# Performance work log

Hardware: AMD Instinct MI355X
Metric: run time of the kernel (lower is better)

Reference implementation:

```python
import jax, jax.numpy as jnp
import numpy as np

N_NODES = 100000


def _sage_conv(x, src, dst, W_l, b_l, W_r):
    # mean-aggregate neighbor (source) features at target nodes
    gathered = x[src]                                   # [E, D]
    summed = jax.ops.segment_sum(gathered, dst, num_segments=N_NODES)  # [N, D]
    deg = jax.ops.segment_sum(jnp.ones((src.shape[0],), x.dtype), dst,
                              num_segments=N_NODES)     # [N]
    mean = summed / jnp.maximum(deg, 1.0)[:, None]      # zero stays zero for isolated nodes
    # PyG SAGEConv: lin_l(aggr) + lin_r(x); bias on lin_l only
    return mean @ W_l + b_l + x @ W_r


def setup_inputs() -> dict:
    key = jax.random.key(0)
    ks = jax.random.split(key, 9)
    x = jax.random.normal(ks[0], (N_NODES, 128), dtype=jnp.float32)
    edge_index = jax.random.randint(ks[1], (2, 1600000), 0, N_NODES, dtype=jnp.int64)
    s1 = 1.0 / np.sqrt(128.0)
    s2 = 1.0 / np.sqrt(32.0)
    return {
        "x": x,
        "edge_index": edge_index,
        "W1_l": jax.random.normal(ks[2], (128, 32), jnp.float32) * s1,
        "b1_l": jax.random.normal(ks[3], (32,), jnp.float32) * s1,
        "W1_r": jax.random.normal(ks[4], (128, 32), jnp.float32) * s1,
        "W2_l": jax.random.normal(ks[5], (32, 32), jnp.float32) * s2,
        "b2_l": jax.random.normal(ks[6], (32,), jnp.float32) * s2,
        "W2_r": jax.random.normal(ks[7], (32, 32), jnp.float32) * s2,
    }


def reference(x, edge_index, W1_l, b1_l, W1_r, W2_l, b2_l, W2_r):
    src, dst = edge_index[0], edge_index[1]
    h = _sage_conv(x, src, dst, W1_l, b1_l, W1_r)
    h = jax.nn.relu(h)
    # dropout is identity in eval mode
    h = _sage_conv(h, src, dst, W2_l, b2_l, W2_r)
    return jax.nn.relu(h)
```

## Files before the change

### kernel.cpp

```cpp
#include <hip/hip_runtime.h>


typedef _Float16 f16;
typedef _Float16 f16x4 __attribute__((ext_vector_type(4)));
typedef _Float16 half8 __attribute__((ext_vector_type(8)));
typedef float f32x4 __attribute__((ext_vector_type(4)));

#define MAXBINS 2048
#define SHIFT 6
#define BINSZ 64
#define CAP 48
#define BSTR 52
#define GBI 3392
#define GSC 256
#define BSC 512
#define SRC_BITS 17
#define SRC_MASK 0x1FFFFu
#define XSTRIDE 136


__global__ __launch_bounds__(256) void gemm_mfma(const float* __restrict__ x,
                                                 const float* __restrict__ Wl,
                                                 const float* __restrict__ Wr,
                                                 f16* __restrict__ yl,
                                                 float* __restrict__ yr,
                                                 int N) {
    __shared__ __align__(16) f16 sX[64 * XSTRIDE];
    __shared__ __align__(16) f16 sWT[64 * XSTRIDE];
    const int tid = threadIdx.x;
    const int row0 = blockIdx.x * 64;

    for (int i = tid; i < 64 * 32; i += 256) {
        int r = i >> 5, c4 = i & 31;
        int row = row0 + r;
        float4 v = make_float4(0.f, 0.f, 0.f, 0.f);
        if (row < N) v = *(const float4*)(x + (size_t)row * 128 + c4 * 4);
        f16* d = &sX[r * XSTRIDE + c4 * 4];
        d[0] = (f16)v.x; d[1] = (f16)v.y; d[2] = (f16)v.z; d[3] = (f16)v.w;
    }
    for (int i = tid; i < 64 * 128; i += 256) {
        int k = i >> 6, n = i & 63;
        float v = (n < 32) ? Wl[k * 32 + n] : Wr[k * 32 + (n - 32)];
        sWT[n * XSTRIDE + k] = (f16)v;
    }
    __syncthreads();

    const int w = tid >> 6;
    const int lane = tid & 63;
    const int l15 = lane & 15, quad = lane >> 4;
    f32x4 acc[4] = {};
#pragma unroll
    for (int kc = 0; kc < 4; ++kc) {
        half8 af = *(const half8*)&sX[(w * 16 + l15) * XSTRIDE + kc * 32 + quad * 8];
#pragma unroll
        for (int nt = 0; nt < 4; ++nt) {
            half8 bf = *(const half8*)&sWT[(nt * 16 + l15) * XSTRIDE + kc * 32 + quad * 8];
            acc[nt] = __builtin_amdgcn_mfma_f32_16x16x32_f16(af, bf, acc[nt], 0, 0, 0);
        }
    }
#pragma unroll
    for (int nt = 0; nt < 4; ++nt) {
        int c = nt * 16 + l15;
#pragma unroll
        for (int r = 0; r < 4; ++r) {
            int g = row0 + w * 16 + quad * 4 + r;
            if (c < 32) yl[(size_t)g * 32 + c] = (f16)acc[nt][r];
            else        yr[(size_t)g * 32 + (c - 32)] = acc[nt][r];
        }
    }
}


__global__ __launch_bounds__(BSC) void scatter_sort(const int* __restrict__ src,
                                                    const int* __restrict__ dst,
                                                    unsigned* __restrict__ pairs,
                                                    unsigned* __restrict__ binSeg,
                                                    int E, int chunk) {
    __shared__ int cnt[MAXBINS];
    __shared__ int wsum[8];
    const int tid = threadIdx.x;
    const int sb = blockIdx.x;
    for (int i = tid; i < MAXBINS; i += BSC) cnt[i] = 0;
    __syncthreads();

    const int base = sb * chunk;
    const int endE = base + chunk < E ? base + chunk : E;
    const int len = endE > base ? endE - base : 0;
    const int nv = len >> 2;
    const int rem = len & 3;
    const int4* s4 = (const int4*)(src + base);
    const int4* d4 = (const int4*)(dst + base);

    for (int i = tid; i < nv; i += BSC) {
        int4 d = d4[i];
        atomicAdd(&cnt[d.x >> SHIFT], 1);
        atomicAdd(&cnt[d.y >> SHIFT], 1);
        atomicAdd(&cnt[d.z >> SHIFT], 1);
        atomicAdd(&cnt[d.w >> SHIFT], 1);
    }
    if (tid < rem) atomicAdd(&cnt[dst[base + nv * 4 + tid] >> SHIFT], 1);
    __syncthreads();

    {
        int b0 = cnt[4 * tid], b1 = cnt[4 * tid + 1],
            b2 = cnt[4 * tid + 2], b3 = cnt[4 * tid + 3];
        int tsum = b0 + b1 + b2 + b3;
        const int lane = tid & 63, wave = tid >> 6;
        int incl = tsum;
#pragma unroll
        for (int off = 1; off < 64; off <<= 1) {
            int t = __shfl_up(incl, off, 64);
            if (lane >= off) incl += t;
        }
        if (lane == 63) wsum[wave] = incl;
        __syncthreads();
        if (tid == 0) {
            int a = 0;
#pragma unroll
            for (int w = 0; w < 8; ++w) { int t = wsum[w]; wsum[w] = a; a += t; }
        }
        __syncthreads();
        int ex = (incl - tsum) + wsum[wave];
        int e0 = ex, e1 = ex + b0, e2 = e1 + b1, e3 = e2 + b2;
        binSeg[(size_t)(4 * tid) * GSC + sb]     = ((unsigned)e0 << 16) | (unsigned)b0;
        binSeg[(size_t)(4 * tid + 1) * GSC + sb] = ((unsigned)e1 << 16) | (unsigned)b1;
        binSeg[(size_t)(4 * tid + 2) * GSC + sb] = ((unsigned)e2 << 16) | (unsigned)b2;
        binSeg[(size_t)(4 * tid + 3) * GSC + sb] = ((unsigned)e3 << 16) | (unsigned)b3;
        __syncthreads();
        cnt[4 * tid] = e0; cnt[4 * tid + 1] = e1;
        cnt[4 * tid + 2] = e2; cnt[4 * tid + 3] = e3;
    }
    __syncthreads();

    unsigned* out = pairs + (size_t)sb * chunk;
    for (int i = tid; i < nv; i += BSC) {
        int4 s = s4[i];
        int4 d = d4[i];
        int slot;
        slot = atomicAdd(&cnt[d.x >> SHIFT], 1);
        out[slot] = ((unsigned)(d.x & (BINSZ - 1)) << SRC_BITS) | (unsigned)s.x;
        slot = atomicAdd(&cnt[d.y >> SHIFT], 1);
        out[slot] = ((unsigned)(d.y & (BINSZ - 1)) << SRC_BITS) | (unsigned)s.y;
        slot = atomicAdd(&cnt[d.z >> SHIFT], 1);
        out[slot] = ((unsigned)(d.z & (BINSZ - 1)) << SRC_BITS) | (unsigned)s.z;
        slot = atomicAdd(&cnt[d.w >> SHIFT], 1);
        out[slot] = ((unsigned)(d.w & (BINSZ - 1)) << SRC_BITS) | (unsigned)s.w;
    }
    if (tid < rem) {
        int e = base + nv * 4 + tid;
        int s = src[e], d = dst[e];
        int slot = atomicAdd(&cnt[d >> SHIFT], 1);
        out[slot] = ((unsigned)(d & (BINSZ - 1)) << SRC_BITS) | (unsigned)s;
    }
}


__device__ __forceinline__ void build_bucket(const unsigned* __restrict__ pairs,
                                             const unsigned* __restrict__ binSeg,
                                             int* sBucket, int* sCnt,
                                             int b, int tid, int chunk) {
    unsigned dsc = binSeg[(size_t)b * GSC + tid];
    int scnt = (int)(dsc & 0xFFFFu);
    const unsigned* p = pairs + (size_t)tid * chunk + (dsc >> 16);
    int k = 0;
    for (; k + 4 <= scnt; k += 4) {
        unsigned p0 = p[k], p1 = p[k + 1], p2 = p[k + 2], p3 = p[k + 3];
        int l, s;
        l = p0 >> SRC_BITS; s = atomicAdd(&sCnt[l], 1);
        if (s < CAP) sBucket[l * BSTR + s] = (int)(p0 & SRC_MASK);
        l = p1 >> SRC_BITS; s = atomicAdd(&sCnt[l], 1);
        if (s < CAP) sBucket[l * BSTR + s] = (int)(p1 & SRC_MASK);
        l = p2 >> SRC_BITS; s = atomicAdd(&sCnt[l], 1);
        if (s < CAP) sBucket[l * BSTR + s] = (int)(p2 & SRC_MASK);
        l = p3 >> SRC_BITS; s = atomicAdd(&sCnt[l], 1);
        if (s < CAP) sBucket[l * BSTR + s] = (int)(p3 & SRC_MASK);
    }
    for (; k < scnt; ++k) {
        unsigned pk = p[k];
        int l = pk >> SRC_BITS;
        int s = atomicAdd(&sCnt[l], 1);
        if (s < CAP) sBucket[l * BSTR + s] = (int)(pk & SRC_MASK);
    }
}

#define PULL8(BKP, TBL, AX)                                                  \
    {                                                                        \
        int4 eA = (BKP)[0], eB = (BKP)[1];                                   \
        half8 v0 = *(const half8*)((TBL) + (size_t)eA.x * 32);               \
        half8 v1 = *(const half8*)((TBL) + (size_t)eA.y * 32);               \
        half8 v2 = *(const half8*)((TBL) + (size_t)eA.z * 32);               \
        half8 v3 = *(const half8*)((TBL) + (size_t)eA.w * 32);               \
        half8 w0 = *(const half8*)((TBL) + (size_t)eB.x * 32);               \
        half8 w1 = *(const half8*)((TBL) + (size_t)eB.y * 32);               \
        half8 w2 = *(const half8*)((TBL) + (size_t)eB.z * 32);               \
        half8 w3 = *(const half8*)((TBL) + (size_t)eB.w * 32);               \
        _Pragma("unroll")                                                    \
        for (int k_ = 0; k_ < 8; ++k_)                                       \
            AX[k_] += (((float)v0[k_] + (float)v1[k_]) +                     \
                       ((float)v2[k_] + (float)v3[k_])) +                    \
                      (((float)w0[k_] + (float)w1[k_]) +                     \
                       ((float)w2[k_] + (float)w3[k_]));                     \
    }

__global__ __launch_bounds__(256, 4) void agg_l1(const unsigned* __restrict__ pairs,
                                                 const unsigned* __restrict__ binSeg,
                                                 int* __restrict__ gB,
                                                 const f16* __restrict__ yl,
                                                 const float* __restrict__ yr,
                                                 const float* __restrict__ b1,
                                                 const float* __restrict__ W2l,
                                                 const float* __restrict__ W2r,
                                                 f16* __restrict__ zl,
                                                 float* __restrict__ zr,
                                                 int N, int chunk) {
    __shared__ __align__(16) int sBucket[BINSZ * BSTR];
    __shared__ __align__(16) int sCnt[BINSZ];
    __shared__ __align__(16) float sW[2048];
    __shared__ __align__(16) float sB[32];
    const int tid = threadIdx.x;
    if (tid < BINSZ) sCnt[tid] = 0;
    if (tid < 32) sB[tid] = b1[tid];
    {
        float4* sW4 = (float4*)sW;
        sW4[tid] = ((const float4*)W2l)[tid];
        sW4[256 + tid] = ((const float4*)W2r)[tid];
        for (int i = tid; i < BINSZ * BSTR; i += 256) sBucket[i] = N;
    }
    __syncthreads();

    const int b = blockIdx.x;
    build_bucket(pairs, binSeg, sBucket, sCnt, b, tid, chunk);
    __syncthreads();

    {
        int4* g4 = (int4*)(gB + (size_t)b * GBI);
        const int4* s4 = (const int4*)sBucket;
        for (int i = tid; i < 832; i += 256) g4[i] = s4[i];
        if (tid < 16) g4[832 + tid] = ((const int4*)sCnt)[tid];
    }

    const int node = tid >> 2;
    const int c8 = tid & 3;
    const int node0 = b << SHIFT;
    const int g = node0 + node;

    float4 locA = *(const float4*)(yr + (size_t)g * 32 + c8 * 8);
    float4 locB = *(const float4*)(yr + (size_t)g * 32 + c8 * 8 + 4);

    const int deg = sCnt[node];
    const int m = deg < CAP ? deg : CAP;
    const int q = (m + 7) >> 3;
    const int4* bk = (const int4*)&sBucket[node * BSTR];
    const float dg = deg > 1 ? (float)deg : 1.0f;

    float ax[8] = {0.f, 0.f, 0.f, 0.f, 0.f, 0.f, 0.f, 0.f};
    {
        const f16* yb = yl + c8 * 8;
        for (int j = 0; j < q; ++j) PULL8(bk + 2 * j, yb, ax);
    }

    float h[8];
    if (g < N) {
        float loc[8];
        *(float4*)&loc[0] = locA;
        *(float4*)&loc[4] = locB;
#pragma unroll
        for (int k = 0; k < 8; ++k)
            h[k] = fmaxf(ax[k] / dg + sB[c8 * 8 + k] + loc[k], 0.0f);
    } else {
#pragma unroll
        for (int k = 0; k < 8; ++k) h[k] = 0.f;
    }
    __syncthreads();

    float* sH = (float*)sBucket;
    *(float4*)&sH[node * 36 + c8 * 8]     = make_float4(h[0], h[1], h[2], h[3]);
    *(float4*)&sH[node * 36 + c8 * 8 + 4] = make_float4(h[4], h[5], h[6], h[7]);
    __syncthreads();

    const int n2 = tid >> 3;
    const int cq = tid & 7;
    const float4* sW4l = (const float4*)sW;
    const float4* sW4r = (const float4*)(sW + 1024);
#pragma unroll
    for (int it = 0; it < 2; ++it) {
        int n = it * 32 + n2;
        int gg = node0 + n;
        float4 al = make_float4(0.f, 0.f, 0.f, 0.f);
        float4 ar = make_float4(0.f, 0.f, 0.f, 0.f);
#pragma unroll 8
        for (int k = 0; k < 32; ++k) {
            float hk = sH[n * 36 + k];
            float4 wl = sW4l[k * 8 + cq];
            float4 wr = sW4r[k * 8 + cq];
            al.x += hk * wl.x; al.y += hk * wl.y; al.z += hk * wl.z; al.w += hk * wl.w;
            ar.x += hk * wr.x; ar.y += hk * wr.y; ar.z += hk * wr.z; ar.w += hk * wr.w;
        }
        f16x4 hh;
        hh[0] = (f16)al.x; hh[1] = (f16)al.y; hh[2] = (f16)al.z; hh[3] = (f16)al.w;
        *(f16x4*)(zl + (size_t)gg * 32 + cq * 4) = hh;
        if (gg < N) *(float4*)(zr + (size_t)gg * 32 + cq * 4) = ar;
    }
}

__global__ __launch_bounds__(256, 4) void agg_l2(const int* __restrict__ gB,
                                                 const f16* __restrict__ zl,
                                                 const float* __restrict__ b2,
                                                 float* __restrict__ io,
                                                 int N) {
    __shared__ __align__(16) int sBucket[BINSZ * BSTR];
    __shared__ __align__(16) int sCnt[BINSZ];
    __shared__ __align__(16) float sB[32];
    const int tid = threadIdx.x;
    if (tid < 32) sB[tid] = b2[tid];

    const int b = blockIdx.x;
    {
        const int4* g4 = (const int4*)(gB + (size_t)b * GBI);
        int4* s4 = (int4*)sBucket;
        for (int i = tid; i < 832; i += 256) s4[i] = g4[i];
        if (tid < 16) ((int4*)sCnt)[tid] = g4[832 + tid];
    }
    __syncthreads();

    const int node = tid >> 2;
    const int c8 = tid & 3;
    const int node0 = b << SHIFT;
    const int g = node0 + node;

    float4 ioA = make_float4(0.f, 0.f, 0.f, 0.f);
    float4 ioB = make_float4(0.f, 0.f, 0.f, 0.f);
    if (g < N) {
        ioA = *(const float4*)(io + (size_t)g * 32 + c8 * 8);
        ioB = *(const float4*)(io + (size_t)g * 32 + c8 * 8 + 4);
    }

    const int deg = sCnt[node];
    const int m = deg < CAP ? deg : CAP;
    const int q = (m + 7) >> 3;
    const int4* bk = (const int4*)&sBucket[node * BSTR];

    float ax[8] = {0.f, 0.f, 0.f, 0.f, 0.f, 0.f, 0.f, 0.f};
    {
        const f16* zb = zl + c8 * 8;
        for (int j = 0; j < q; ++j) PULL8(bk + 2 * j, zb, ax);
    }

    if (g < N) {
        float dg = deg > 1 ? (float)deg : 1.0f;
        float v[8];
        *(float4*)&v[0] = ioA;
        *(float4*)&v[4] = ioB;
        float o[8];
#pragma unroll
        for (int k = 0; k < 8; ++k)
            o[k] = fmaxf(ax[k] / dg + sB[c8 * 8 + k] + v[k], 0.0f);
        *(float4*)(io + (size_t)g * 32 + c8 * 8)     = *(float4*)&o[0];
        *(float4*)(io + (size_t)g * 32 + c8 * 8 + 4) = *(float4*)&o[4];
    }
}

extern "C" void kernel_launch(void* const* d_in, const int* in_sizes, int n_in,
                              void* d_out, int out_size, void* d_ws, size_t ws_size,
                              hipStream_t stream) {
    const float* x    = (const float*)d_in[0];
    const int*   ei   = (const int*)d_in[1];
    const float* W1l  = (const float*)d_in[2];
    const float* b1l  = (const float*)d_in[3];
    const float* W1r  = (const float*)d_in[4];
    const float* W2l  = (const float*)d_in[5];
    const float* b2l  = (const float*)d_in[6];
    const float* W2r  = (const float*)d_in[7];

    const int N = in_sizes[0] / 128;
    const int E = in_sizes[1] / 2;
    const int* srcIdx = ei;
    const int* dstIdx = ei + E;

    const int gridG = (N >> 6) + 1;
    const int NP = gridG << 6;

    const int nbins = (N + BINSZ - 1) >> SHIFT;
    const int chunk = (((E + GSC - 1) / GSC) + 3) & ~3;

    unsigned* binSeg = (unsigned*)d_ws;
    unsigned* pairs  = binSeg + (size_t)MAXBINS * GSC;
    f16*      A      = (f16*)(pairs + (size_t)GSC * chunk);
    float*    B      = (float*)(A + (size_t)NP * 32);
    f16*      Z      = (f16*)(B + (size_t)NP * 32);
    int*      gB     = (int*)(Z + (size_t)NP * 32);
    float*    outp   = (float*)d_out;

    gemm_mfma<<<gridG, 256, 0, stream>>>(x, W1l, W1r, A, B, N);
    scatter_sort<<<GSC, BSC, 0, stream>>>(srcIdx, dstIdx, pairs, binSeg, E, chunk);
    agg_l1<<<nbins, 256, 0, stream>>>(pairs, binSeg, gB, A, B, b1l,
                                      W2l, W2r, Z, outp, N, chunk);
    agg_l2<<<nbins, 256, 0, stream>>>(gB, Z, b2l, outp, N);
}
```

Baseline: 190.6 us.

## Replace two-level bin sort with direct global-atomic bucket scatter

The shared-memory counting sort into bins, and the per-block bucket build in agg_l1, are replaced by a single kernel that does global atomicAdd on per-node degree counters and writes each source index straight into a fixed-capacity per-node bucket in global memory. The degree array is zeroed inside the GEMM kernel, and both aggregation kernels load their buckets directly, padding with a sentinel index. This removes the pairs/binSeg intermediate, one kernel's worth of passes, and the bucket write-back from agg_l1. In exchange it relies on 1.6M contended global atomics with scattered 4-byte writes, which may have poor locality.

```diff
diff --git a/kernel.cpp b/kernel.cpp
--- a/kernel.cpp
+++ b/kernel.cpp
@@ -6,16 +6,11 @@
 typedef _Float16 half8 __attribute__((ext_vector_type(8)));
 typedef float f32x4 __attribute__((ext_vector_type(4)));
 
-#define MAXBINS 2048
 #define SHIFT 6
 #define BINSZ 64
 #define CAP 48
 #define BSTR 52
-#define GBI 3392
-#define GSC 256
-#define BSC 512
-#define SRC_BITS 17
-#define SRC_MASK 0x1FFFFu
+#define SDG 1024
 #define XSTRIDE 136
 
 
@@ -24,11 +19,17 @@
                                                  const float* __restrict__ Wr,
                                                  f16* __restrict__ yl,
                                                  float* __restrict__ yr,
-                                                 int N) {
+                                                 int* __restrict__ deg,
+                                                 int N, int nDeg) {
     __shared__ __align__(16) f16 sX[64 * XSTRIDE];
     __shared__ __align__(16) f16 sWT[64 * XSTRIDE];
     const int tid = threadIdx.x;
     const int row0 = blockIdx.x * 64;
+
+    {
+        int gi = blockIdx.x * 256 + tid;
+        if (gi < nDeg) deg[gi] = 0;
+    }
 
     for (int i = tid; i < 64 * 32; i += 256) {
         int r = i >> 5, c4 = i & 31;
@@ -71,116 +72,55 @@
 }
 
 
-__global__ __launch_bounds__(BSC) void scatter_sort(const int* __restrict__ src,
-                                                    const int* __restrict__ dst,
-                                                    unsigned* __restrict__ pairs,
-                                                    unsigned* __restrict__ binSeg,
-                                                    int E, int chunk) {
-    __shared__ int cnt[MAXBINS];
-    __shared__ int wsum[8];
-    const int tid = threadIdx.x;
-    const int sb = blockIdx.x;
-    for (int i = tid; i < MAXBINS; i += BSC) cnt[i] = 0;
-    __syncthreads();
-
-    const int base = sb * chunk;
-    const int endE = base + chunk < E ? base + chunk : E;
-    const int len = endE > base ? endE - base : 0;
-    const int nv = len >> 2;
-    const int rem = len & 3;
-    const int4* s4 = (const int4*)(src + base);
-    const int4* d4 = (const int4*)(dst + base);
-
-    for (int i = tid; i < nv; i += BSC) {
-        int4 d = d4[i];
-        atomicAdd(&cnt[d.x >> SHIFT], 1);
-        atomicAdd(&cnt[d.y >> SHIFT], 1);
-        atomicAdd(&cnt[d.z >> SHIFT], 1);
-        atomicAdd(&cnt[d.w >> SHIFT], 1);
-    }
-    if (tid < rem) atomicAdd(&cnt[dst[base + nv * 4 + tid] >> SHIFT], 1);
-    __syncthreads();
-
-    {
-        int b0 = cnt[4 * tid], b1 = cnt[4 * tid + 1],
-            b2 = cnt[4 * tid + 2], b3 = cnt[4 * tid + 3];
-        int tsum = b0 + b1 + b2 + b3;
-        const int lane = tid & 63, wave = tid >> 6;
-        int incl = tsum;
-#pragma unroll
-        for (int off = 1; off < 64; off <<= 1) {
-            int t = __shfl_up(incl, off, 64);
-            if (lane >= off) incl += t;
-        }
-        if (lane == 63) wsum[wave] = incl;
-        __syncthreads();
-        if (tid == 0) {
-            int a = 0;
-#pragma unroll
-            for (int w = 0; w < 8; ++w) { int t = wsum[w]; wsum[w] = a; a += t; }
-        }
-        __syncthreads();
-        int ex = (incl - tsum) + wsum[wave];
-        int e0 = ex, e1 = ex + b0, e2 = e1 + b1, e3 = e2 + b2;
-        binSeg[(size_t)(4 * tid) * GSC + sb]     = ((unsigned)e0 << 16) | (unsigned)b0;
-        binSeg[(size_t)(4 * tid + 1) * GSC + sb] = ((unsigned)e1 << 16) | (unsigned)b1;
-        binSeg[(size_t)(4 * tid + 2) * GSC + sb] = ((unsigned)e2 << 16) | (unsigned)b2;
-        binSeg[(size_t)(4 * tid + 3) * GSC + sb] = ((unsigned)e3 << 16) | (unsigned)b3;
-        __syncthreads();
-        cnt[4 * tid] = e0; cnt[4 * tid + 1] = e1;
-        cnt[4 * tid + 2] = e2; cnt[4 * tid + 3] = e3;
-    }
-    __syncthreads();
-
-    unsigned* out = pairs + (size_t)sb * chunk;
-    for (int i = tid; i < nv; i += BSC) {
+__global__ __launch_bounds__(256) void scatter_direct(const int* __restrict__ src,
+                                                      const int* __restrict__ dst,
+                                                      int* __restrict__ deg,
+                                                      int* __restrict__ gBkt,
+                                                      int E) {
+    const int nv = E >> 2;
+    const int4* s4 = (const int4*)src;
+    const int4* d4 = (const int4*)dst;
+    const int idx = blockIdx.x * 256 + threadIdx.x;
+    const int stride = gridDim.x * 256;
+    for (int i = idx; i < nv; i += stride) {
         int4 s = s4[i];
         int4 d = d4[i];
         int slot;
-        slot = atomicAdd(&cnt[d.x >> SHIFT], 1);
-        out[slot] = ((unsigned)(d.x & (BINSZ - 1)) << SRC_BITS) | (unsigned)s.x;
-        slot = atomicAdd(&cnt[d.y >> SHIFT], 1);
-        out[slot] = ((unsigned)(d.y & (BINSZ - 1)) << SRC_BITS) | (unsigned)s.y;
-        slot = atomicAdd(&cnt[d.z >> SHIFT], 1);
-        out[slot] = ((unsigned)(d.z & (BINSZ - 1)) << SRC_BITS) | (unsigned)s.z;
-        slot = atomicAdd(&cnt[d.w >> SHIFT], 1);
-        out[slot] = ((unsigned)(d.w & (BINSZ - 1)) << SRC_BITS) | (unsigned)s.w;
-    }
-    if (tid < rem) {
-        int e = base + nv * 4 + tid;
+        slot = atomicAdd(&deg[d.x], 1);
+        if (slot < CAP) gBkt[d.x * BSTR + slot] = s.x;
+        slot = atomicAdd(&deg[d.y], 1);
+        if (slot < CAP) gBkt[d.y * BSTR + slot] = s.y;
+        slot = atomicAdd(&deg[d.z], 1);
+        if (slot < CAP) gBkt[d.z * BSTR + slot] = s.z;
+        slot = atomicAdd(&deg[d.w], 1);
+        if (slot < CAP) gBkt[d.w * BSTR + slot] = s.w;
+    }
+    const int rem = E & 3;
+    if (idx < rem) {
+        int e = nv * 4 + idx;
         int s = src[e], d = dst[e];
-        int slot = atomicAdd(&cnt[d >> SHIFT], 1);
-        out[slot] = ((unsigned)(d & (BINSZ - 1)) << SRC_BITS) | (unsigned)s;
-    }
-}
-
-
-__device__ __forceinline__ void build_bucket(const unsigned* __restrict__ pairs,
-                                             const unsigned* __restrict__ binSeg,
-                                             int* sBucket, int* sCnt,
-                                             int b, int tid, int chunk) {
-    unsigned dsc = binSeg[(size_t)b * GSC + tid];
-    int scnt = (int)(dsc & 0xFFFFu);
-    const unsigned* p = pairs + (size_t)tid * chunk + (dsc >> 16);
-    int k = 0;
-    for (; k + 4 <= scnt; k += 4) {
-        unsigned p0 = p[k], p1 = p[k + 1], p2 = p[k + 2], p3 = p[k + 3];
-        int l, s;
-        l = p0 >> SRC_BITS; s = atomicAdd(&sCnt[l], 1);
-        if (s < CAP) sBucket[l * BSTR + s] = (int)(p0 & SRC_MASK);
-        l = p1 >> SRC_BITS; s = atomicAdd(&sCnt[l], 1);
-        if (s < CAP) sBucket[l * BSTR + s] = (int)(p1 & SRC_MASK);
-        l = p2 >> SRC_BITS; s = atomicAdd(&sCnt[l], 1);
-        if (s < CAP) sBucket[l * BSTR + s] = (int)(p2 & SRC_MASK);
-        l = p3 >> SRC_BITS; s = atomicAdd(&sCnt[l], 1);
-        if (s < CAP) sBucket[l * BSTR + s] = (int)(p3 & SRC_MASK);
-    }
-    for (; k < scnt; ++k) {
-        unsigned pk = p[k];
-        int l = pk >> SRC_BITS;
-        int s = atomicAdd(&sCnt[l], 1);
-        if (s < CAP) sBucket[l * BSTR + s] = (int)(pk & SRC_MASK);
-    }
+        int slot = atomicAdd(&deg[d], 1);
+        if (slot < CAP) gBkt[d * BSTR + slot] = s;
+    }
+}
+
+
+__device__ __forceinline__ void load_bucket(const int* __restrict__ gBkt,
+                                            const int* __restrict__ deg,
+                                            int* sBucket, int* sCnt,
+                                            int b, int tid, int N) {
+    const int4* g4 = (const int4*)(gBkt + (size_t)b * (BINSZ * BSTR));
+    int4* s4 = (int4*)sBucket;
+    for (int i = tid; i < BINSZ * BSTR / 4; i += 256) s4[i] = g4[i];
+    if (tid < BINSZ / 4) ((int4*)sCnt)[tid] = ((const int4*)(deg + b * BINSZ))[tid];
+    __syncthreads();
+    if (tid < BINSZ) {
+        int c = sCnt[tid];
+        int m = c < CAP ? c : CAP;
+        int mp = (m + 7) & ~7;
+        for (int k = m; k < mp; ++k) sBucket[tid * BSTR + k] = N;
+    }
+    __syncthreads();
 }
 
 #define PULL8(BKP, TBL, AX)                                                  \
@@ -202,9 +142,8 @@
                        ((float)w2[k_] + (float)w3[k_]));                     \
     }
 
-__global__ __launch_bounds__(256, 4) void agg_l1(const unsigned* __restrict__ pairs,
-                                                 const unsigned* __restrict__ binSeg,
-                                                 int* __restrict__ gB,
+__global__ __launch_bounds__(256, 4) void agg_l1(const int* __restrict__ gBkt,
+                                                 const int* __restrict__ deg,
                                                  const f16* __restrict__ yl,
                                                  const float* __restrict__ yr,
                                                  const float* __restrict__ b1,
@@ -212,32 +151,21 @@
                                                  const float* __restrict__ W2r,
                                                  f16* __restrict__ zl,
                                                  float* __restrict__ zr,
-                                                 int N, int chunk) {
+                                                 int N) {
     __shared__ __align__(16) int sBucket[BINSZ * BSTR];
     __shared__ __align__(16) int sCnt[BINSZ];
     __shared__ __align__(16) float sW[2048];
     __shared__ __align__(16) float sB[32];
     const int tid = threadIdx.x;
-    if (tid < BINSZ) sCnt[tid] = 0;
     if (tid < 32) sB[tid] = b1[tid];
     {
         float4* sW4 = (float4*)sW;
         sW4[tid] = ((const float4*)W2l)[tid];
         sW4[256 + tid] = ((const float4*)W2r)[tid];
-        for (int i = tid; i < BINSZ * BSTR; i += 256) sBucket[i] = N;
-    }
-    __syncthreads();
+    }
 
     const int b = blockIdx.x;
-    build_bucket(pairs, binSeg, sBucket, sCnt, b, tid, chunk);
-    __syncthreads();
-
-    {
-        int4* g4 = (int4*)(gB + (size_t)b * GBI);
-        const int4* s4 = (const int4*)sBucket;
-        for (int i = tid; i < 832; i += 256) g4[i] = s4[i];
-        if (tid < 16) g4[832 + tid] = ((const int4*)sCnt)[tid];
-    }
+    load_bucket(gBkt, deg, sBucket, sCnt, b, tid, N);
 
     const int node = tid >> 2;
     const int c8 = tid & 3;
@@ -247,11 +175,11 @@
     float4 locA = *(const float4*)(yr + (size_t)g * 32 + c8 * 8);
     float4 locB = *(const float4*)(yr + (size_t)g * 32 + c8 * 8 + 4);
 
-    const int deg = sCnt[node];
-    const int m = deg < CAP ? deg : CAP;
+    const int dgi = sCnt[node];
+    const int m = dgi < CAP ? dgi : CAP;
     const int q = (m + 7) >> 3;
     const int4* bk = (const int4*)&sBucket[node * BSTR];
-    const float dg = deg > 1 ? (float)deg : 1.0f;
+    const float dg = dgi > 1 ? (float)dgi : 1.0f;
 
     float ax[8] = {0.f, 0.f, 0.f, 0.f, 0.f, 0.f, 0.f, 0.f};
     {
@@ -303,7 +231,8 @@
     }
 }
 
-__global__ __launch_bounds__(256, 4) void agg_l2(const int* __restrict__ gB,
+__global__ __launch_bounds__(256, 4) void agg_l2(const int* __restrict__ gBkt,
+                                                 const int* __restrict__ deg,
                                                  const f16* __restrict__ zl,
                                                  const float* __restrict__ b2,
                                                  float* __restrict__ io,
@@ -315,13 +244,7 @@
     if (tid < 32) sB[tid] = b2[tid];
 
     const int b = blockIdx.x;
-    {
-        const int4* g4 = (const int4*)(gB + (size_t)b * GBI);
-        int4* s4 = (int4*)sBucket;
-        for (int i = tid; i < 832; i += 256) s4[i] = g4[i];
-        if (tid < 16) ((int4*)sCnt)[tid] = g4[832 + tid];
-    }
-    __syncthreads();
+    load_bucket(gBkt, deg, sBucket, sCnt, b, tid, N);
 
     const int node = tid >> 2;
     const int c8 = tid & 3;
@@ -335,8 +258,8 @@
         ioB = *(const float4*)(io + (size_t)g * 32 + c8 * 8 + 4);
     }
 
-    const int deg = sCnt[node];
-    const int m = deg < CAP ? deg : CAP;
+    const int dgi = sCnt[node];
+    const int m = dgi < CAP ? dgi : CAP;
     const int q = (m + 7) >> 3;
     const int4* bk = (const int4*)&sBucket[node * BSTR];
 
@@ -347,7 +270,7 @@
     }
 
     if (g < N) {
-        float dg = deg > 1 ? (float)deg : 1.0f;
+        float dg = dgi > 1 ? (float)dgi : 1.0f;
         float v[8];
         *(float4*)&v[0] = ioA;
         *(float4*)&v[4] = ioB;
@@ -379,21 +302,18 @@
 
     const int gridG = (N >> 6) + 1;
     const int NP = gridG << 6;
-
     const int nbins = (N + BINSZ - 1) >> SHIFT;
-    const int chunk = (((E + GSC - 1) / GSC) + 3) & ~3;
-
-    unsigned* binSeg = (unsigned*)d_ws;
-    unsigned* pairs  = binSeg + (size_t)MAXBINS * GSC;
-    f16*      A      = (f16*)(pairs + (size_t)GSC * chunk);
-    float*    B      = (float*)(A + (size_t)NP * 32);
-    f16*      Z      = (f16*)(B + (size_t)NP * 32);
-    int*      gB     = (int*)(Z + (size_t)NP * 32);
-    float*    outp   = (float*)d_out;
-
-    gemm_mfma<<<gridG, 256, 0, stream>>>(x, W1l, W1r, A, B, N);
-    scatter_sort<<<GSC, BSC, 0, stream>>>(srcIdx, dstIdx, pairs, binSeg, E, chunk);
-    agg_l1<<<nbins, 256, 0, stream>>>(pairs, binSeg, gB, A, B, b1l,
-                                      W2l, W2r, Z, outp, N, chunk);
-    agg_l2<<<nbins, 256, 0, stream>>>(gB, Z, b2l, outp, N);
-}
+
+    int*   deg  = (int*)d_ws;
+    int*   gBkt = deg + NP;
+    f16*   A    = (f16*)(gBkt + (size_t)NP * BSTR);
+    float* B    = (float*)(A + (size_t)NP * 32);
+    f16*   Z    = (f16*)(B + (size_t)NP * 32);
+    float* outp = (float*)d_out;
+
+    gemm_mfma<<<gridG, 256, 0, stream>>>(x, W1l, W1r, A, B, deg, N, NP);
+    scatter_direct<<<SDG, 256, 0, stream>>>(srcIdx, dstIdx, deg, gBkt, E);
+    agg_l1<<<nbins, 256, 0, stream>>>(gBkt, deg, A, B, b1l,
+                                      W2l, W2r, Z, outp, N);
+    agg_l2<<<nbins, 256, 0, stream>>>(gBkt, deg, Z, b2l, outp, N);
+}
```

Result: slower. 294.3 us (+54.4%).

## Merge GEMM and edge scatter-sort into one heterogeneous prep kernel

Applied to the files above, without the earlier changes.

Combines the layer-1 MFMA GEMM and the edge bucketing scatter_sort into a single launch, where the first 256 blocks do the scatter-sort and the rest do GEMM tiles. The aim is to run the two independent stages concurrently on the GPU and drop one launch boundary. To fit the shared GEMM block shape, the scatter blocks shrink from 512 to 256 threads, so each thread scans 8 bins instead of 4. The cost is less parallelism per sort block and a larger shared-memory footprint, since the union allocation may lower occupancy for the sort path.

```diff
diff --git a/kernel.cpp b/kernel.cpp
--- a/kernel.cpp
+++ b/kernel.cpp
@@ -13,22 +13,110 @@
 #define BSTR 52
 #define GBI 3392
 #define GSC 256
-#define BSC 512
 #define SRC_BITS 17
 #define SRC_MASK 0x1FFFFu
 #define XSTRIDE 136
 
 
-__global__ __launch_bounds__(256) void gemm_mfma(const float* __restrict__ x,
-                                                 const float* __restrict__ Wl,
-                                                 const float* __restrict__ Wr,
-                                                 f16* __restrict__ yl,
-                                                 float* __restrict__ yr,
-                                                 int N) {
-    __shared__ __align__(16) f16 sX[64 * XSTRIDE];
-    __shared__ __align__(16) f16 sWT[64 * XSTRIDE];
+__global__ __launch_bounds__(256) void prep(const float* __restrict__ x,
+                                            const float* __restrict__ Wl,
+                                            const float* __restrict__ Wr,
+                                            const int* __restrict__ src,
+                                            const int* __restrict__ dst,
+                                            unsigned* __restrict__ pairs,
+                                            unsigned* __restrict__ binSeg,
+                                            f16* __restrict__ yl,
+                                            float* __restrict__ yr,
+                                            int N, int E, int chunk) {
+    __shared__ __align__(16) f16 smem[2 * 64 * XSTRIDE];
     const int tid = threadIdx.x;
-    const int row0 = blockIdx.x * 64;
+
+    if ((int)blockIdx.x < GSC) {
+        int* cnt = (int*)smem;
+        __shared__ int wsum[4];
+        for (int i = tid; i < MAXBINS; i += 256) cnt[i] = 0;
+        __syncthreads();
+
+        const int sb = blockIdx.x;
+        const int base = sb * chunk;
+        const int endE = base + chunk < E ? base + chunk : E;
+        const int len = endE > base ? endE - base : 0;
+        const int nv = len >> 2;
+        const int rem = len & 3;
+        const int4* s4 = (const int4*)(src + base);
+        const int4* d4 = (const int4*)(dst + base);
+
+        for (int i = tid; i < nv; i += 256) {
+            int4 d = d4[i];
+            atomicAdd(&cnt[d.x >> SHIFT], 1);
+            atomicAdd(&cnt[d.y >> SHIFT], 1);
+            atomicAdd(&cnt[d.z >> SHIFT], 1);
+            atomicAdd(&cnt[d.w >> SHIFT], 1);
+        }
+        if (tid < rem) atomicAdd(&cnt[dst[base + nv * 4 + tid] >> SHIFT], 1);
+        __syncthreads();
+
+        {
+            int bv[8];
+            int tsum = 0;
+#pragma unroll
+            for (int j = 0; j < 8; ++j) { bv[j] = cnt[8 * tid + j]; tsum += bv[j]; }
+            const int lane = tid & 63, wave = tid >> 6;
+            int incl = tsum;
+#pragma unroll
+            for (int off = 1; off < 64; off <<= 1) {
+                int t = __shfl_up(incl, off, 64);
+                if (lane >= off) incl += t;
+            }
+            if (lane == 63) wsum[wave] = incl;
+            __syncthreads();
+            if (tid == 0) {
+                int a = 0;
+#pragma unroll
+                for (int w = 0; w < 4; ++w) { int t = wsum[w]; wsum[w] = a; a += t; }
+            }
+            __syncthreads();
+            int ex = (incl - tsum) + wsum[wave];
+            int e[8];
+            e[0] = ex;
+#pragma unroll
+            for (int j = 1; j < 8; ++j) e[j] = e[j - 1] + bv[j - 1];
+#pragma unroll
+            for (int j = 0; j < 8; ++j)
+                binSeg[(size_t)(8 * tid + j) * GSC + sb] =
+                    ((unsigned)e[j] << 16) | (unsigned)bv[j];
+            __syncthreads();
+#pragma unroll
+            for (int j = 0; j < 8; ++j) cnt[8 * tid + j] = e[j];
+        }
+        __syncthreads();
+
+        unsigned* out = pairs + (size_t)sb * chunk;
+        for (int i = tid; i < nv; i += 256) {
+            int4 s = s4[i];
+            int4 d = d4[i];
+            int slot;
+            slot = atomicAdd(&cnt[d.x >> SHIFT], 1);
+            out[slot] = ((unsigned)(d.x & (BINSZ - 1)) << SRC_BITS) | (unsigned)s.x;
+            slot = atomicAdd(&cnt[d.y >> SHIFT], 1);
+            out[slot] = ((unsigned)(d.y & (BINSZ - 1)) << SRC_BITS) | (unsigned)s.y;
+            slot = atomicAdd(&cnt[d.z >> SHIFT], 1);
+            out[slot] = ((unsigned)(d.z & (BINSZ - 1)) << SRC_BITS) | (unsigned)s.z;
+            slot = atomicAdd(&cnt[d.w >> SHIFT], 1);
+            out[slot] = ((unsigned)(d.w & (BINSZ - 1)) << SRC_BITS) | (unsigned)s.w;
+        }
+        if (tid < rem) {
+            int e = base + nv * 4 + tid;
+            int s = src[e], d = dst[e];
+            int slot = atomicAdd(&cnt[d >> SHIFT], 1);
+            out[slot] = ((unsigned)(d & (BINSZ - 1)) << SRC_BITS) | (unsigned)s;
+        }
+        return;
+    }
+
+    f16* sX = smem;
+    f16* sWT = smem + 64 * XSTRIDE;
+    const int row0 = (blockIdx.x - GSC) * 64;
 
     for (int i = tid; i < 64 * 32; i += 256) {
         int r = i >> 5, c4 = i & 31;
@@ -67,90 +155,6 @@
             if (c < 32) yl[(size_t)g * 32 + c] = (f16)acc[nt][r];
             else        yr[(size_t)g * 32 + (c - 32)] = acc[nt][r];
         }
-    }
-}
-
-
-__global__ __launch_bounds__(BSC) void scatter_sort(const int* __restrict__ src,
-                                                    const int* __restrict__ dst,
-                                                    unsigned* __restrict__ pairs,
-                                                    unsigned* __restrict__ binSeg,
-                                                    int E, int chunk) {
-    __shared__ int cnt[MAXBINS];
-    __shared__ int wsum[8];
-    const int tid = threadIdx.x;
-    const int sb = blockIdx.x;
-    for (int i = tid; i < MAXBINS; i += BSC) cnt[i] = 0;
-    __syncthreads();
-
-    const int base = sb * chunk;
-    const int endE = base + chunk < E ? base + chunk : E;
-    const int len = endE > base ? endE - base : 0;
-    const int nv = len >> 2;
-    const int rem = len & 3;
-    const int4* s4 = (const int4*)(src + base);
-    const int4* d4 = (const int4*)(dst + base);
-
-    for (int i = tid; i < nv; i += BSC) {
-        int4 d = d4[i];
-        atomicAdd(&cnt[d.x >> SHIFT], 1);
-        atomicAdd(&cnt[d.y >> SHIFT], 1);
-        atomicAdd(&cnt[d.z >> SHIFT], 1);
-        atomicAdd(&cnt[d.w >> SHIFT], 1);
-    }
-    if (tid < rem) atomicAdd(&cnt[dst[base + nv * 4 + tid] >> SHIFT], 1);
-    __syncthreads();
-
-    {
-        int b0 = cnt[4 * tid], b1 = cnt[4 * tid + 1],
-            b2 = cnt[4 * tid + 2], b3 = cnt[4 * tid + 3];
-        int tsum = b0 + b1 + b2 + b3;
-        const int lane = tid & 63, wave = tid >> 6;
-        int incl = tsum;
-#pragma unroll
-        for (int off = 1; off < 64; off <<= 1) {
-            int t = __shfl_up(incl, off, 64);
-            if (lane >= off) incl += t;
-        }
-        if (lane == 63) wsum[wave] = incl;
-        __syncthreads();
-        if (tid == 0) {
-            int a = 0;
-#pragma unroll
-            for (int w = 0; w < 8; ++w) { int t = wsum[w]; wsum[w] = a; a += t; }
-        }
-        __syncthreads();
-        int ex = (incl - tsum) + wsum[wave];
-        int e0 = ex, e1 = ex + b0, e2 = e1 + b1, e3 = e2 + b2;
-        binSeg[(size_t)(4 * tid) * GSC + sb]     = ((unsigned)e0 << 16) | (unsigned)b0;
-        binSeg[(size_t)(4 * tid + 1) * GSC + sb] = ((unsigned)e1 << 16) | (unsigned)b1;
-        binSeg[(size_t)(4 * tid + 2) * GSC + sb] = ((unsigned)e2 << 16) | (unsigned)b2;
-        binSeg[(size_t)(4 * tid + 3) * GSC + sb] = ((unsigned)e3 << 16) | (unsigned)b3;
-        __syncthreads();
-        cnt[4 * tid] = e0; cnt[4 * tid + 1] = e1;
-        cnt[4 * tid + 2] = e2; cnt[4 * tid + 3] = e3;
-    }
-    __syncthreads();
-
-    unsigned* out = pairs + (size_t)sb * chunk;
-    for (int i = tid; i < nv; i += BSC) {
-        int4 s = s4[i];
-        int4 d = d4[i];
-        int slot;
-        slot = atomicAdd(&cnt[d.x >> SHIFT], 1);
-        out[slot] = ((unsigned)(d.x & (BINSZ - 1)) << SRC_BITS) | (unsigned)s.x;
-        slot = atomicAdd(&cnt[d.y >> SHIFT], 1);
-        out[slot] = ((unsigned)(d.y & (BINSZ - 1)) << SRC_BITS) | (unsigned)s.y;
-        slot = atomicAdd(&cnt[d.z >> SHIFT], 1);
-        out[slot] = ((unsigned)(d.z & (BINSZ - 1)) << SRC_BITS) | (unsigned)s.z;
-        slot = atomicAdd(&cnt[d.w >> SHIFT], 1);
-        out[slot] = ((unsigned)(d.w & (BINSZ - 1)) << SRC_BITS) | (unsigned)s.w;
-    }
-    if (tid < rem) {
-        int e = base + nv * 4 + tid;
-        int s = src[e], d = dst[e];
-        int slot = atomicAdd(&cnt[d >> SHIFT], 1);
-        out[slot] = ((unsigned)(d & (BINSZ - 1)) << SRC_BITS) | (unsigned)s;
     }
 }
 
@@ -247,11 +251,11 @@
     float4 locA = *(const float4*)(yr + (size_t)g * 32 + c8 * 8);
     float4 locB = *(const float4*)(yr + (size_t)g * 32 + c8 * 8 + 4);
 
-    const int deg = sCnt[node];
-    const int m = deg < CAP ? deg : CAP;
+    const int dgi = sCnt[node];
+    const int m = dgi < CAP ? dgi : CAP;
     const int q = (m + 7) >> 3;
     const int4* bk = (const int4*)&sBucket[node * BSTR];
-    const float dg = deg > 1 ? (float)deg : 1.0f;
+    const float dg = dgi > 1 ? (float)dgi : 1.0f;
 
     float ax[8] = {0.f, 0.f, 0.f, 0.f, 0.f, 0.f, 0.f, 0.f};
     {
@@ -335,8 +339,8 @@
         ioB = *(const float4*)(io + (size_t)g * 32 + c8 * 8 + 4);
     }
 
-    const int deg = sCnt[node];
-    const int m = deg < CAP ? deg : CAP;
+    const int dgi = sCnt[node];
+    const int m = dgi < CAP ? dgi : CAP;
     const int q = (m + 7) >> 3;
     const int4* bk = (const int4*)&sBucket[node * BSTR];
 
@@ -347,7 +351,7 @@
     }
 
     if (g < N) {
-        float dg = deg > 1 ? (float)deg : 1.0f;
+        float dg = dgi > 1 ? (float)dgi : 1.0f;
         float v[8];
         *(float4*)&v[0] = ioA;
         *(float4*)&v[4] = ioB;
@@ -391,8 +395,8 @@
     int*      gB     = (int*)(Z + (size_t)NP * 32);
     float*    outp   = (float*)d_out;
 
-    gemm_mfma<<<gridG, 256, 0, stream>>>(x, W1l, W1r, A, B, N);
-    scatter_sort<<<GSC, BSC, 0, stream>>>(srcIdx, dstIdx, pairs, binSeg, E, chunk);
+    prep<<<GSC + gridG, 256, 0, stream>>>(x, W1l, W1r, srcIdx, dstIdx,
+                                          pairs, binSeg, A, B, N, E, chunk);
     agg_l1<<<nbins, 256, 0, stream>>>(pairs, binSeg, gB, A, B, b1l,
                                       W2l, W2r, Z, outp, N, chunk);
     agg_l2<<<nbins, 256, 0, stream>>>(gB, Z, b2l, outp, N);
```

Result: faster. 186.3 us (-2.3%).
